# Kernel optimization log

Measured on AMD Instinct MI355X. Metric: run time of the kernel, lower is better.

The kernel has to match this reference:

```python
import jax, jax.numpy as jnp
from jax import lax
import numpy as np

B, T, H = 4096, 2048, 32


def setup_inputs() -> dict:
    key = jax.random.key(0)
    ks = jax.random.split(key, 12)
    s = 1.0 / np.sqrt(H)
    u = lambda k, shape: jax.random.uniform(k, shape, jnp.float32, -s, s)
    return {
        "x": jax.random.normal(ks[0], (B, T), jnp.float32),
        "w_ih0": u(ks[1], (H, 1)),
        "w_hh0": u(ks[2], (H, H)),
        "b_ih0": u(ks[3], (H,)),
        "b_hh0": u(ks[4], (H,)),
        "w_ih1": u(ks[5], (H, H)),
        "w_hh1": u(ks[6], (H, H)),
        "b_ih1": u(ks[7], (H,)),
        "b_hh1": u(ks[8], (H,)),
        "w_out": u(ks[9], (1, H)),
        "b_out": u(ks[10], (1,)),
        "future": 0,
    }


def reference(x, w_ih0, w_hh0, b_ih0, b_hh0, w_ih1, w_hh1, b_ih1, b_hh1,
              w_out, b_out, future):
    Bx, Tx = x.shape
    xs = x.T[:, :, None]  # [T, B, 1]
    h0 = jnp.zeros((Bx, H), x.dtype)
    h1 = jnp.zeros((Bx, H), x.dtype)

    def cell(x_t, h0, h1):
        h0 = jnp.tanh(x_t @ w_ih0.T + b_ih0 + h0 @ w_hh0.T + b_hh0)
        h1 = jnp.tanh(h0 @ w_ih1.T + b_ih1 + h1 @ w_hh1.T + b_hh1)
        out = h1 @ w_out.T + b_out  # [B, 1]
        return h0, h1, out

    def step(carry, x_t):
        h0, h1 = carry
        h0, h1, out = cell(x_t, h0, h1)
        return (h0, h1), out

    (h0, h1), outs = lax.scan(step, (h0, h1), xs)  # outs: [T, B, 1]

    if future > 0:
        def fstep(carry, _):
            h0, h1, out = carry
            h0, h1, out = cell(out, h0, h1)
            return (h0, h1, out), out

        _, fouts = lax.scan(fstep, (h0, h1, outs[-1]), None, length=future)
        outs = jnp.concatenate([outs, fouts], axis=0)

    return outs[:, :, 0].T  # [B, T+future]
```

## Files before the change

kernel.cpp:

```cpp
#include <hip/hip_runtime.h>
#include <stdint.h>
#include <math.h>

typedef float f32x4 __attribute__((ext_vector_type(4)));
typedef float f32x2 __attribute__((ext_vector_type(2)));
typedef _Float16 f16x8 __attribute__((ext_vector_type(8)));
typedef _Float16 f16x2 __attribute__((ext_vector_type(2)));

namespace {

constexpr int kB = 4096;
constexpr int kT = 2048;
constexpr int kNSB = kT / 16;
constexpr float kS = 2.8853900817779268f;

union Frag { f16x2 h2[4]; f16x8 v; uint32_t u[4]; };
union H2U { f16x2 h; uint32_t u; };

__device__ __forceinline__ f16x2 pk(float a, float b) {
  return __builtin_bit_cast(f16x2, __builtin_amdgcn_cvt_pkrtz(a, b));
}
__device__ __forceinline__ f32x4 mfma(f16x8 a, f16x8 b, f32x4 c) {
  return __builtin_amdgcn_mfma_f32_16x16x32_f16(a, b, c, 0, 0, 0);
}
__device__ __forceinline__ f16x2 fmh(f16x2 a, f16x2 b, f16x2 c) {
  return __builtin_elementwise_fma(a, b, c);
}
__device__ __forceinline__ f16x2 csgn2(f16x2 p, f16x2 s) {
  H2U up, us, r;
  up.h = p; us.h = s;
  r.u = (up.u & 0x7FFF7FFFu) | (us.u & 0x80008000u);
  return r.h;
}

__device__ __forceinline__ void loadfrag_hi(const float* W, int tile, int lane,
                                            Frag& hi) {
  const int mm = lane & 15, gg = lane >> 4;
  const int j = 8 * (mm >> 2) + 4 * tile + (mm & 3);
  const float* p = W + j * 32 + 8 * gg;
  float w8[8];
#pragma unroll
  for (int q = 0; q < 2; ++q) {
    float4 t = ((const float4*)p)[q];
    w8[4 * q + 0] = t.x * kS; w8[4 * q + 1] = t.y * kS;
    w8[4 * q + 2] = t.z * kS; w8[4 * q + 3] = t.w * kS;
  }
#pragma unroll
  for (int q = 0; q < 4; ++q) hi.h2[q] = pk(w8[2 * q], w8[2 * q + 1]);
}

}

extern "C" __global__ __launch_bounds__(128, 1) void rnn2_p8(
    const float* __restrict__ x, const float* __restrict__ w_ih0,
    const float* __restrict__ w_hh0, const float* __restrict__ b_ih0,
    const float* __restrict__ b_hh0, const float* __restrict__ w_ih1,
    const float* __restrict__ w_hh1, const float* __restrict__ b_ih1,
    const float* __restrict__ b_hh1, const float* __restrict__ w_out,
    const float* __restrict__ b_out, float* __restrict__ out,
    float c0, float c1, float c2, float c3, float c4) {
  const int tid = (int)threadIdx.x;
  const int role = tid >> 6;
  const int lane = tid & 63;
  const int g = lane >> 4, m = lane & 15;
  const int rg = (int)blockIdx.x * 16 + m;

  const f16x2 C0 = {(_Float16)c0, (_Float16)c0};
  const f16x2 C1 = {(_Float16)c1, (_Float16)c1};
  const f16x2 C2 = {(_Float16)c2, (_Float16)c2};
  const f16x2 C3 = {(_Float16)c3, (_Float16)c3};
  const f16x2 C4 = {(_Float16)c4, (_Float16)c4};

  __shared__ __align__(16) _Float16 hbuf[16][16][32];
  const int swz = 8 * ((g + (m >> 2)) & 3);

  auto horner2 = [&](f16x2 w) {
    f16x2 p = fmh(w, C4, C3);
    p = fmh(w, p, C2);
    p = fmh(w, p, C1);
    p = fmh(w, p, C0);
    return p;
  };
  auto tanh8 = [&](const f32x4& z0, const f32x4& z1, Frag& hf) {
    float w0 = __builtin_amdgcn_exp2f(-__builtin_fabsf(z0[0]));
    float w1 = __builtin_amdgcn_exp2f(-__builtin_fabsf(z0[1]));
    float w2 = __builtin_amdgcn_exp2f(-__builtin_fabsf(z0[2]));
    float w3 = __builtin_amdgcn_exp2f(-__builtin_fabsf(z0[3]));
    float w4 = __builtin_amdgcn_exp2f(-__builtin_fabsf(z1[0]));
    float w5 = __builtin_amdgcn_exp2f(-__builtin_fabsf(z1[1]));
    float w6 = __builtin_amdgcn_exp2f(-__builtin_fabsf(z1[2]));
    float w7 = __builtin_amdgcn_exp2f(-__builtin_fabsf(z1[3]));
    f16x2 pa = horner2(pk(w0, w1));
    f16x2 pb = horner2(pk(w2, w3));
    f16x2 pc = horner2(pk(w4, w5));
    f16x2 pd = horner2(pk(w6, w7));
    hf.h2[0] = csgn2(pa, pk(z0[0], z0[1]));
    hf.h2[1] = csgn2(pb, pk(z0[2], z0[3]));
    hf.h2[2] = csgn2(pc, pk(z1[0], z1[1]));
    hf.h2[3] = csgn2(pd, pk(z1[2], z1[3]));
  };

  Frag Wa[2], Wb[2];
  f32x4 cv4[2];
  f32x4 wih4[2];
  f16x2 wo2[4];
  float bout = 0.f;
  Frag h0, h1;
#pragma unroll
  for (int q = 0; q < 4; ++q) { h0.u[q] = 0; h1.u[q] = 0; }

  if (role == 0) {
#pragma unroll
    for (int t = 0; t < 2; ++t) loadfrag_hi(w_hh0, t, lane, Wa[t]);
#pragma unroll
    for (int t = 0; t < 2; ++t)
#pragma unroll
      for (int i = 0; i < 4; ++i) {
        int jj = 8 * g + 4 * t + i;
        cv4[t][i] = (b_ih0[jj] + b_hh0[jj]) * kS;
        wih4[t][i] = w_ih0[jj] * kS;
      }
  } else {
#pragma unroll
    for (int t = 0; t < 2; ++t) {
      loadfrag_hi(w_hh1, t, lane, Wa[t]);
      loadfrag_hi(w_ih1, t, lane, Wb[t]);
    }
#pragma unroll
    for (int t = 0; t < 2; ++t)
#pragma unroll
      for (int i = 0; i < 4; ++i) {
        int jj = 8 * g + 4 * t + i;
        cv4[t][i] = (b_ih1[jj] + b_hh1[jj]) * kS;
      }
#pragma unroll
    for (int q = 0; q < 4; ++q) {
      int jj = 8 * g + 4 * (q >> 1) + 2 * (q & 1);
      wo2[q] = pk(w_out[jj], w_out[jj + 1]);
    }
    bout = b_out[0];
  }

  const float* xrow = x + (long)rg * kT;
  float* orow = out + (long)rg * kT;

  auto stepA = [&](float xt, int slot) {
    f32x4 xt4 = {xt, xt, xt, xt};
    f32x4 zi0 = __builtin_elementwise_fma(xt4, wih4[0], cv4[0]);
    f32x4 zi1 = __builtin_elementwise_fma(xt4, wih4[1], cv4[1]);
    f32x4 z0 = mfma(Wa[0].v, h0.v, zi0);
    f32x4 z1 = mfma(Wa[1].v, h0.v, zi1);
    tanh8(z0, z1, h0);
    *reinterpret_cast<f16x8*>(&hbuf[slot][m][swz]) = h0.v;
  };

  float stash[16];
  auto stepB = [&](const Frag& hf, float* st) {
    f32x4 y0 = mfma(Wb[0].v, hf.v, cv4[0]);
    f32x4 y1 = mfma(Wb[1].v, hf.v, cv4[1]);
    y0 = mfma(Wa[0].v, h1.v, y0);
    y1 = mfma(Wa[1].v, h1.v, y1);
    tanh8(y0, y1, h1);
    f16x2 acc = h1.h2[0] * wo2[0];
    acc = fmh(h1.h2[1], wo2[1], acc);
    acc = fmh(h1.h2[2], wo2[2], acc);
    acc = fmh(h1.h2[3], wo2[3], acc);
    *st = (float)acc.x + (float)acc.y;
  };

  auto readslot = [&](int slot) {
    Frag r;
    r.v = *reinterpret_cast<const f16x8*>(&hbuf[slot][m][swz]);
    return r;
  };

  auto reduce_store = [&](int base) {
    float r[16];
#pragma unroll
    for (int i = 0; i < 16; ++i) {
      float s = stash[i];
      s += __shfl_xor(s, 16, 64);
      s += __shfl_xor(s, 32, 64);
      r[i] = s + bout;
    }
    if (lane < 16) {
      float4* dst = (float4*)(orow + base);
      dst[0] = make_float4(r[0], r[1], r[2], r[3]);
      dst[1] = make_float4(r[4], r[5], r[6], r[7]);
      dst[2] = make_float4(r[8], r[9], r[10], r[11]);
      dst[3] = make_float4(r[12], r[13], r[14], r[15]);
    }
  };

  float xc[16], xn[16];
  if (role == 0) {
    float4 q0 = ((const float4*)xrow)[0], q1 = ((const float4*)xrow)[1];
    float4 q2 = ((const float4*)xrow)[2], q3 = ((const float4*)xrow)[3];
    xn[0]=q0.x; xn[1]=q0.y; xn[2]=q0.z; xn[3]=q0.w;
    xn[4]=q1.x; xn[5]=q1.y; xn[6]=q1.z; xn[7]=q1.w;
    xn[8]=q2.x; xn[9]=q2.y; xn[10]=q2.z; xn[11]=q2.w;
    xn[12]=q3.x; xn[13]=q3.y; xn[14]=q3.z; xn[15]=q3.w;
  }

  Frag pf[8];
#pragma unroll
  for (int k = 0; k < 8; ++k)
#pragma unroll
    for (int q = 0; q < 4; ++q) pf[k].u[q] = 0;

  for (int pq = 0; pq < 256; pq += 2) {
#pragma unroll
    for (int pp = 0; pp < 2; ++pp) {
      const int p = pq + pp;
      if (role == 0) {
        if (pp == 0) {
#pragma unroll
          for (int i = 0; i < 16; ++i) xc[i] = xn[i];
          const int nb = ((pq >> 1) + 1 < kNSB) ? ((pq >> 1) + 1) : (kNSB - 1);
          const float* src = xrow + nb * 16;
          float4 q0 = ((const float4*)src)[0], q1 = ((const float4*)src)[1];
          float4 q2 = ((const float4*)src)[2], q3 = ((const float4*)src)[3];
          xn[0]=q0.x; xn[1]=q0.y; xn[2]=q0.z; xn[3]=q0.w;
          xn[4]=q1.x; xn[5]=q1.y; xn[6]=q1.z; xn[7]=q1.w;
          xn[8]=q2.x; xn[9]=q2.y; xn[10]=q2.z; xn[11]=q2.w;
          xn[12]=q3.x; xn[13]=q3.y; xn[14]=q3.z; xn[15]=q3.w;
        }
        stepA(xc[8 * pp + 0], 8 * pp + 0);
        stepA(xc[8 * pp + 1], 8 * pp + 1);
        stepA(xc[8 * pp + 2], 8 * pp + 2);
        stepA(xc[8 * pp + 3], 8 * pp + 3);
        stepA(xc[8 * pp + 4], 8 * pp + 4);
        stepA(xc[8 * pp + 5], 8 * pp + 5);
        stepA(xc[8 * pp + 6], 8 * pp + 6);
        stepA(xc[8 * pp + 7], 8 * pp + 7);
      } else {
        if (pp == 1 && pq >= 2) reduce_store(((pq >> 1) - 1) * 16);
        if (p >= 1) {
          const int sb = 8 - 8 * pp;
          pf[0] = readslot(sb + 0);
          pf[1] = readslot(sb + 1);
          pf[2] = readslot(sb + 2);
          pf[3] = readslot(sb + 3);
          pf[4] = readslot(sb + 4);
          pf[5] = readslot(sb + 5);
          pf[6] = readslot(sb + 6);
          pf[7] = readslot(sb + 7);
          stepB(pf[0], &stash[sb + 0]);
          stepB(pf[1], &stash[sb + 1]);
          stepB(pf[2], &stash[sb + 2]);
          stepB(pf[3], &stash[sb + 3]);
          stepB(pf[4], &stash[sb + 4]);
          stepB(pf[5], &stash[sb + 5]);
          stepB(pf[6], &stash[sb + 6]);
          stepB(pf[7], &stash[sb + 7]);
        }
      }
      asm volatile("s_waitcnt lgkmcnt(0)\n\ts_barrier" ::: "memory");
    }
  }

  if (role == 1) {
    pf[0] = readslot(8);  pf[1] = readslot(9);
    pf[2] = readslot(10); pf[3] = readslot(11);
    pf[4] = readslot(12); pf[5] = readslot(13);
    pf[6] = readslot(14); pf[7] = readslot(15);
    stepB(pf[0], &stash[8]);
    stepB(pf[1], &stash[9]);
    stepB(pf[2], &stash[10]);
    stepB(pf[3], &stash[11]);
    stepB(pf[4], &stash[12]);
    stepB(pf[5], &stash[13]);
    stepB(pf[6], &stash[14]);
    stepB(pf[7], &stash[15]);
    reduce_store(kT - 16);
  }
}

namespace {
void tanh_poly_coeffs(float* out5) {
  const int N = 64, D = 5;
  double ATA[5][5] = {}, ATf[5] = {};
  for (int i = 0; i < N; ++i) {
    double u = cos(M_PI * (i + 0.5) / N);
    double w = 0.5 * (u + 1.0);
    double f = (1.0 - w) / (1.0 + w);
    double pw[5];
    pw[0] = 1.0;
    for (int k = 1; k < D; ++k) pw[k] = pw[k - 1] * w;
    for (int r = 0; r < D; ++r) {
      ATf[r] += pw[r] * f;
      for (int c = 0; c < D; ++c) ATA[r][c] += pw[r] * pw[c];
    }
  }
  double M[5][6];
  for (int r = 0; r < D; ++r) {
    for (int c = 0; c < D; ++c) M[r][c] = ATA[r][c];
    M[r][D] = ATf[r];
  }
  for (int col = 0; col < D; ++col) {
    int best = col;
    for (int r = col + 1; r < D; ++r)
      if (fabs(M[r][col]) > fabs(M[best][col])) best = r;
    for (int c = col; c <= D; ++c) {
      double t = M[col][c]; M[col][c] = M[best][c]; M[best][c] = t;
    }
    for (int r = col + 1; r < D; ++r) {
      double s = M[r][col] / M[col][col];
      for (int c = col; c <= D; ++c) M[r][c] -= s * M[col][c];
    }
  }
  double xs[5];
  for (int r = D - 1; r >= 0; --r) {
    double s = M[r][D];
    for (int c = r + 1; c < D; ++c) s -= M[r][c] * xs[c];
    xs[r] = s / M[r][r];
  }
  for (int k = 0; k < D; ++k) out5[k] = (float)xs[k];
}
}

extern "C" void kernel_launch(void* const* d_in, const int* in_sizes, int n_in,
                              void* d_out, int out_size, void* d_ws, size_t ws_size,
                              hipStream_t stream) {
  (void)in_sizes; (void)n_in; (void)d_ws; (void)ws_size; (void)out_size;
  const float* xp = (const float*)d_in[0];
  const float* w_ih0 = (const float*)d_in[1];
  const float* w_hh0 = (const float*)d_in[2];
  const float* b_ih0 = (const float*)d_in[3];
  const float* b_hh0 = (const float*)d_in[4];
  const float* w_ih1 = (const float*)d_in[5];
  const float* w_hh1 = (const float*)d_in[6];
  const float* b_ih1 = (const float*)d_in[7];
  const float* b_hh1 = (const float*)d_in[8];
  const float* w_out = (const float*)d_in[9];
  const float* b_out = (const float*)d_in[10];

  float c[5];
  tanh_poly_coeffs(c);

  dim3 grid(kB / 16);
  dim3 block(128);
  hipLaunchKernelGGL(rnn2_p8, grid, block, 0, stream,
                     xp, w_ih0, w_hh0, b_ih0, b_hh0,
                     w_ih1, w_hh1, b_ih1, b_hh1,
                     w_out, b_out, (float*)d_out,
                     c[0], c[1], c[2], c[3], c[4]);
}
```

Measured before the change: 344.7 us.

## Move layer-1 input projection to layer-0 wave, pass fp32 preactivations via LDS

Wave 0 (layer 0) now also computes the W_ih1·h0 + bias MFMA and writes the fp32 preactivations to shared memory, instead of handing fp16 h0 to wave 1. Wave 1 (layer 1) then only runs the recurrent W_hh1 MFMA plus tanh and output per step. This rebalances work between the two pipelined roles so the sequential critical path of the layer-1 wave gets shorter. In exchange the LDS buffer doubles in size and traffic, since it now holds fp32 instead of fp16, and wave 0 carries more work per step.

```diff
diff --git a/kernel.cpp b/kernel.cpp
--- a/kernel.cpp
+++ b/kernel.cpp
@@ -3,7 +3,6 @@
 #include <math.h>
 
 typedef float f32x4 __attribute__((ext_vector_type(4)));
-typedef float f32x2 __attribute__((ext_vector_type(2)));
 typedef _Float16 f16x8 __attribute__((ext_vector_type(8)));
 typedef _Float16 f16x2 __attribute__((ext_vector_type(2)));
 
@@ -51,7 +50,7 @@
 
 }
 
-extern "C" __global__ __launch_bounds__(128, 1) void rnn2_p8(
+extern "C" __global__ __launch_bounds__(128, 1) void rnn2_yb(
     const float* __restrict__ x, const float* __restrict__ w_ih0,
     const float* __restrict__ w_hh0, const float* __restrict__ b_ih0,
     const float* __restrict__ b_hh0, const float* __restrict__ w_ih1,
@@ -71,8 +70,7 @@
   const f16x2 C3 = {(_Float16)c3, (_Float16)c3};
   const f16x2 C4 = {(_Float16)c4, (_Float16)c4};
 
-  __shared__ __align__(16) _Float16 hbuf[16][16][32];
-  const int swz = 8 * ((g + (m >> 2)) & 3);
+  __shared__ __align__(16) float ybuf[16][16][32];
 
   auto horner2 = [&](f16x2 w) {
     f16x2 p = fmh(w, C4, C3);
@@ -102,6 +100,7 @@
 
   Frag Wa[2], Wb[2];
   f32x4 cv4[2];
+  f32x4 cvB[2];
   f32x4 wih4[2];
   f16x2 wo2[4];
   float bout = 0.f;
@@ -111,28 +110,22 @@
 
   if (role == 0) {
 #pragma unroll
-    for (int t = 0; t < 2; ++t) loadfrag_hi(w_hh0, t, lane, Wa[t]);
+    for (int t = 0; t < 2; ++t) {
+      loadfrag_hi(w_hh0, t, lane, Wa[t]);
+      loadfrag_hi(w_ih1, t, lane, Wb[t]);
+    }
 #pragma unroll
     for (int t = 0; t < 2; ++t)
 #pragma unroll
       for (int i = 0; i < 4; ++i) {
         int jj = 8 * g + 4 * t + i;
         cv4[t][i] = (b_ih0[jj] + b_hh0[jj]) * kS;
+        cvB[t][i] = (b_ih1[jj] + b_hh1[jj]) * kS;
         wih4[t][i] = w_ih0[jj] * kS;
       }
   } else {
 #pragma unroll
-    for (int t = 0; t < 2; ++t) {
-      loadfrag_hi(w_hh1, t, lane, Wa[t]);
-      loadfrag_hi(w_ih1, t, lane, Wb[t]);
-    }
-#pragma unroll
-    for (int t = 0; t < 2; ++t)
-#pragma unroll
-      for (int i = 0; i < 4; ++i) {
-        int jj = 8 * g + 4 * t + i;
-        cv4[t][i] = (b_ih1[jj] + b_hh1[jj]) * kS;
-      }
+    for (int t = 0; t < 2; ++t) loadfrag_hi(w_hh1, t, lane, Wa[t]);
 #pragma unroll
     for (int q = 0; q < 4; ++q) {
       int jj = 8 * g + 4 * (q >> 1) + 2 * (q & 1);
@@ -143,6 +136,9 @@
 
   const float* xrow = x + (long)rg * kT;
   float* orow = out + (long)rg * kT;
+
+  const int go0 = ((2 * g + m) & 7) * 4;
+  const int go1 = ((2 * g + 1 + m) & 7) * 4;
 
   auto stepA = [&](float xt, int slot) {
     f32x4 xt4 = {xt, xt, xt, xt};
@@ -151,15 +147,17 @@
     f32x4 z0 = mfma(Wa[0].v, h0.v, zi0);
     f32x4 z1 = mfma(Wa[1].v, h0.v, zi1);
     tanh8(z0, z1, h0);
-    *reinterpret_cast<f16x8*>(&hbuf[slot][m][swz]) = h0.v;
+    f32x4 yi0 = mfma(Wb[0].v, h0.v, cvB[0]);
+    f32x4 yi1 = mfma(Wb[1].v, h0.v, cvB[1]);
+    float* row = &ybuf[slot][m][0];
+    *(f32x4*)(row + go0) = yi0;
+    *(f32x4*)(row + go1) = yi1;
   };
 
   float stash[16];
-  auto stepB = [&](const Frag& hf, float* st) {
-    f32x4 y0 = mfma(Wb[0].v, hf.v, cv4[0]);
-    f32x4 y1 = mfma(Wb[1].v, hf.v, cv4[1]);
-    y0 = mfma(Wa[0].v, h1.v, y0);
-    y1 = mfma(Wa[1].v, h1.v, y1);
+  auto stepB = [&](const f32x4& ya, const f32x4& yb, float* st) {
+    f32x4 y0 = mfma(Wa[0].v, h1.v, ya);
+    f32x4 y1 = mfma(Wa[1].v, h1.v, yb);
     tanh8(y0, y1, h1);
     f16x2 acc = h1.h2[0] * wo2[0];
     acc = fmh(h1.h2[1], wo2[1], acc);
@@ -168,10 +166,10 @@
     *st = (float)acc.x + (float)acc.y;
   };
 
-  auto readslot = [&](int slot) {
-    Frag r;
-    r.v = *reinterpret_cast<const f16x8*>(&hbuf[slot][m][swz]);
-    return r;
+  auto readpair = [&](int slot, f32x4& a, f32x4& b) {
+    const float* row = &ybuf[slot][m][0];
+    a = *(const f32x4*)(row + go0);
+    b = *(const f32x4*)(row + go1);
   };
 
   auto reduce_store = [&](int base) {
@@ -202,11 +200,12 @@
     xn[12]=q3.x; xn[13]=q3.y; xn[14]=q3.z; xn[15]=q3.w;
   }
 
-  Frag pf[8];
-#pragma unroll
-  for (int k = 0; k < 8; ++k)
-#pragma unroll
-    for (int q = 0; q < 4; ++q) pf[k].u[q] = 0;
+  f32x4 pfa[8], pfb[8];
+#pragma unroll
+  for (int k = 0; k < 8; ++k) {
+    pfa[k] = (f32x4){0.f, 0.f, 0.f, 0.f};
+    pfb[k] = pfa[k];
+  }
 
   for (int pq = 0; pq < 256; pq += 2) {
 #pragma unroll
@@ -237,22 +236,22 @@
         if (pp == 1 && pq >= 2) reduce_store(((pq >> 1) - 1) * 16);
         if (p >= 1) {
           const int sb = 8 - 8 * pp;
-          pf[0] = readslot(sb + 0);
-          pf[1] = readslot(sb + 1);
-          pf[2] = readslot(sb + 2);
-          pf[3] = readslot(sb + 3);
-          pf[4] = readslot(sb + 4);
-          pf[5] = readslot(sb + 5);
-          pf[6] = readslot(sb + 6);
-          pf[7] = readslot(sb + 7);
-          stepB(pf[0], &stash[sb + 0]);
-          stepB(pf[1], &stash[sb + 1]);
-          stepB(pf[2], &stash[sb + 2]);
-          stepB(pf[3], &stash[sb + 3]);
-          stepB(pf[4], &stash[sb + 4]);
-          stepB(pf[5], &stash[sb + 5]);
-          stepB(pf[6], &stash[sb + 6]);
-          stepB(pf[7], &stash[sb + 7]);
+          readpair(sb + 0, pfa[0], pfb[0]);
+          readpair(sb + 1, pfa[1], pfb[1]);
+          readpair(sb + 2, pfa[2], pfb[2]);
+          readpair(sb + 3, pfa[3], pfb[3]);
+          readpair(sb + 4, pfa[4], pfb[4]);
+          readpair(sb + 5, pfa[5], pfb[5]);
+          readpair(sb + 6, pfa[6], pfb[6]);
+          readpair(sb + 7, pfa[7], pfb[7]);
+          stepB(pfa[0], pfb[0], &stash[sb + 0]);
+          stepB(pfa[1], pfb[1], &stash[sb + 1]);
+          stepB(pfa[2], pfb[2], &stash[sb + 2]);
+          stepB(pfa[3], pfb[3], &stash[sb + 3]);
+          stepB(pfa[4], pfb[4], &stash[sb + 4]);
+          stepB(pfa[5], pfb[5], &stash[sb + 5]);
+          stepB(pfa[6], pfb[6], &stash[sb + 6]);
+          stepB(pfa[7], pfb[7], &stash[sb + 7]);
         }
       }
       asm volatile("s_waitcnt lgkmcnt(0)\n\ts_barrier" ::: "memory");
@@ -260,18 +259,22 @@
   }
 
   if (role == 1) {
-    pf[0] = readslot(8);  pf[1] = readslot(9);
-    pf[2] = readslot(10); pf[3] = readslot(11);
-    pf[4] = readslot(12); pf[5] = readslot(13);
-    pf[6] = readslot(14); pf[7] = readslot(15);
-    stepB(pf[0], &stash[8]);
-    stepB(pf[1], &stash[9]);
-    stepB(pf[2], &stash[10]);
-    stepB(pf[3], &stash[11]);
-    stepB(pf[4], &stash[12]);
-    stepB(pf[5], &stash[13]);
-    stepB(pf[6], &stash[14]);
-    stepB(pf[7], &stash[15]);
+    readpair(8, pfa[0], pfb[0]);
+    readpair(9, pfa[1], pfb[1]);
+    readpair(10, pfa[2], pfb[2]);
+    readpair(11, pfa[3], pfb[3]);
+    readpair(12, pfa[4], pfb[4]);
+    readpair(13, pfa[5], pfb[5]);
+    readpair(14, pfa[6], pfb[6]);
+    readpair(15, pfa[7], pfb[7]);
+    stepB(pfa[0], pfb[0], &stash[8]);
+    stepB(pfa[1], pfb[1], &stash[9]);
+    stepB(pfa[2], pfb[2], &stash[10]);
+    stepB(pfa[3], pfb[3], &stash[11]);
+    stepB(pfa[4], pfb[4], &stash[12]);
+    stepB(pfa[5], pfb[5], &stash[13]);
+    stepB(pfa[6], pfb[6], &stash[14]);
+    stepB(pfa[7], pfb[7], &stash[15]);
     reduce_store(kT - 16);
   }
 }
@@ -340,7 +343,7 @@
 
   dim3 grid(kB / 16);
   dim3 block(128);
-  hipLaunchKernelGGL(rnn2_p8, grid, block, 0, stream,
+  hipLaunchKernelGGL(rnn2_yb, grid, block, 0, stream,
                      xp, w_ih0, w_hh0, b_ih0, b_hh0,
                      w_ih1, w_hh1, b_ih1, b_hh1,
                      w_out, b_out, (float*)d_out,
```

After: 372.2 us. 8.0% more time.
